# Optimization experiments

Hardware: AMD Instinct MI355X
Metric: run time of the kernel (lower is better)

The kernel has to match this reference:

```python
import jax, jax.numpy as jnp
import numpy as np

N, E, C, LMAX, NELEM = 20000, 400000, 64, 3, 10
AVG_NEIGH = 20.0


def setup_inputs() -> dict:
    key = jax.random.key(0)
    ks = jax.random.split(key, 8)
    elems = jax.random.randint(ks[0], (N,), 0, NELEM)
    node_attrs = jax.nn.one_hot(elems, NELEM, dtype=jnp.float32)  # one-hot element encoding (argmax'd by skip_tp)
    node_feats = jax.random.normal(ks[1], (N, C), dtype=jnp.float32)
    edge_attrs = jax.random.normal(ks[2], (E, (LMAX + 1) ** 2), dtype=jnp.float32)  # spherical harmonics Y_lm, lmax=3 -> 16
    edge_feats = jax.random.normal(ks[3], (E, (LMAX + 1) * C), dtype=jnp.float32)  # radial (spline) features, viewed [E, lmax+1, C]
    W_up = jax.random.normal(ks[4], (C, C), dtype=jnp.float32) / np.float32(np.sqrt(C))  # linear_matmul (pre-normalized)
    W_lin = jax.random.normal(ks[5], (LMAX + 1, C, C), dtype=jnp.float32) / np.float32(np.sqrt(C))  # per-l Linear
    W_skip = jax.random.normal(ks[6], (NELEM, LMAX + 1, C, C), dtype=jnp.float32) / np.float32(np.sqrt(C * NELEM))  # ElementalLinear
    sender = jax.random.randint(ks[7], (E,), 0, N)
    receiver = jax.random.randint(jax.random.fold_in(key, 123), (E,), 0, N)
    edge_index = jnp.stack([sender, receiver]).astype(jnp.int32)
    return dict(node_attrs=node_attrs, node_feats=node_feats, edge_attrs=edge_attrs,
                edge_feats=edge_feats, W_up=W_up, W_lin=W_lin, W_skip=W_skip,
                edge_index=edge_index)


def reference(node_attrs, node_feats, edge_attrs, edge_feats, W_up, W_lin, W_skip, edge_index):
    """InvariantInteraction of OptimizedScaleShiftInvariantMACE:
    linear_up -> InvariantMessagePassingTP (gather/TP/scatter) -> per-l linear / avg_num_neighbors
    -> elemental skip linear selected by node element (one-hot node_attrs)."""
    sender, receiver = edge_index[0], edge_index[1]
    n_nodes = node_feats.shape[0]
    n_edges = edge_feats.shape[0]

    nf = node_feats @ W_up                                   # [N, C] linear up
    ef = edge_feats.reshape(n_edges, LMAX + 1, -1)           # [E, lmax+1, C]
    sf = nf[sender]                                          # [E, C] gather sender feats

    outs = []
    for l in range(LMAX + 1):  # fixed small loop over l-blocks (structurally distinct irreps)
        sh = edge_attrs[:, l * l:(l + 1) * (l + 1)]          # [E, 2l+1]
        # per-edge tensor product: Y_lm(e) * R_l(e,c) * h(sender(e),c)
        m = sh[:, :, None] * (sf * ef[:, l, :])[:, None, :]  # [E, 2l+1, C]
        msg = jax.ops.segment_sum(m, receiver, num_segments=n_nodes)  # [N, 2l+1, C]
        msg = jnp.einsum('nmc,cd->nmd', msg, W_lin[l]) / AVG_NEIGH    # message linear
        Weff = jnp.einsum('nz,zcd->ncd', node_attrs, W_skip[:, l])    # per-node element weights
        outs.append(jnp.einsum('nmc,ncd->nmd', msg, Weff))            # elemental skip linear
    return jnp.concatenate(outs, axis=1)                     # [N, (lmax+1)^2, C]
```

## Files before the change

### kernel.cpp

```cpp
#include <hip/hip_runtime.h>

#define N_NODES 20000
#define N_EDGES 400000
#define NELEM 10
#define INV_AVG (1.0f / 20.0f)
#define NUP_BLK 5000
#define CAP 64

typedef __attribute__((ext_vector_type(8))) short short8;
typedef __attribute__((ext_vector_type(4))) float f32x4;

__device__ __forceinline__ int rlanei(int v, int l) {
    return __builtin_amdgcn_readlane(v, l);
}
__device__ __forceinline__ ushort f2bf(float x) {
    unsigned u = __float_as_uint(x);
    u += 0x7FFFu + ((u >> 16) & 1u);
    return (ushort)(u >> 16);
}
__device__ __forceinline__ float bf2f(ushort h) {
    return __uint_as_float(((unsigned)h) << 16);
}
__host__ __device__ constexpr int lOf(int lm) {
    return lm >= 9 ? 3 : lm >= 4 ? 2 : lm >= 1 ? 1 : 0;
}

__global__ void __launch_bounds__(256) k_prep(
    const float* __restrict__ node_feats,
    const float* __restrict__ W_up,
    const float* __restrict__ W_lin,
    const float* __restrict__ W_skip,
    float* __restrict__ nf,
    ushort* __restrict__ Wfrag)
{
    __shared__ float A[64 * 64];
    __shared__ float B[64 * 64];
    __shared__ float Cw[64 * 64];
    int tid = threadIdx.x;
    if (blockIdx.x < NUP_BLK) {
        for (int i = tid; i < 4096; i += 256) A[i] = W_up[i];
        __syncthreads();
        int n = blockIdx.x * 4 + (tid >> 6);
        int c = tid & 63;
        const float* row = node_feats + (size_t)n * 64;
        float acc = 0.f;
#pragma unroll
        for (int k = 0; k < 64; ++k) acc += row[k] * A[k * 64 + c];
        nf[(size_t)n * 64 + c] = acc;
    } else {
        int zl = blockIdx.x - NUP_BLK;
        int l = zl & 3;
        for (int i = tid; i < 4096; i += 256) {
            A[i] = W_lin[l * 4096 + i];
            B[i] = W_skip[zl * 4096 + i];
        }
        __syncthreads();
        for (int i = tid; i < 4096; i += 256) {
            int k = i >> 6, d = i & 63;
            float acc = 0.f;
#pragma unroll
            for (int c = 0; c < 64; ++c) acc += A[k * 64 + c] * B[c * 64 + d];
            Cw[i] = acc * INV_AVG;
        }
        __syncthreads();
        for (int fid = tid; fid < 8192; fid += 256) {
            int plane = fid >> 12;
            int rem = fid & 4095;
            int kk = rem >> 11;
            int nt = (rem >> 9) & 3;
            int ln = (rem >> 3) & 63;
            int j  = rem & 7;
            int c = kk * 32 + ((ln >> 4) << 3) + j;
            int d = nt * 16 + (ln & 15);
            float v = Cw[c * 64 + d];
            ushort hi = f2bf(v);
            ushort val = plane ? f2bf(v - bf2f(hi)) : hi;
            Wfrag[(size_t)plane * 163840 + (((size_t)zl * 2 + kk) * 4 + nt) * 512 + ln * 8 + j] = val;
        }
    }
}

__global__ void __launch_bounds__(256) k_bucket(
    const int* __restrict__ sender, const int* __restrict__ receiver,
    int* __restrict__ cnt, int2* __restrict__ slots)
{
    int e = blockIdx.x * 256 + threadIdx.x;
    if (e >= N_EDGES) return;
    int r = receiver[e];
    int p = atomicAdd(&cnt[r], 1);
    if (p < CAP) slots[(size_t)r * CAP + p] = make_int2(e, sender[e]);
}

struct Slot {
    float f0, f1, f2, f3, sh, sf;
};

__device__ __forceinline__ void refill(
    Slot& S, int eb, int sb, int idx, int lane,
    const float* __restrict__ edge_feats,
    const float* __restrict__ edge_attrs,
    const float* __restrict__ nf)
{
    int e_ = rlanei(eb, idx);
    int s_ = rlanei(sb, idx);
    const float* ef_ = edge_feats + (size_t)e_ * 256;
    S.f0 = ef_[lane];
    S.f1 = ef_[64 + lane];
    S.f2 = ef_[128 + lane];
    S.f3 = ef_[192 + lane];
    S.sh = edge_attrs[(size_t)e_ * 16 + (lane & 15)];
    S.sf = nf[(size_t)s_ * 64 + lane];
}

__device__ __forceinline__ float rlanef(float v, int l) {
    return __int_as_float(__builtin_amdgcn_readlane(__float_as_int(v), l));
}

__device__ __forceinline__ void compute(const Slot& S, float* acc)
{
    float pr0 = S.sf * S.f0, pr1 = S.sf * S.f1;
    float pr2 = S.sf * S.f2, pr3 = S.sf * S.f3;
    acc[0] += rlanef(S.sh, 0) * pr0;
#pragma unroll
    for (int lm = 1; lm < 4; ++lm)  acc[lm] += rlanef(S.sh, lm) * pr1;
#pragma unroll
    for (int lm = 4; lm < 9; ++lm)  acc[lm] += rlanef(S.sh, lm) * pr2;
#pragma unroll
    for (int lm = 9; lm < 16; ++lm) acc[lm] += rlanef(S.sh, lm) * pr3;
}

__global__ void __launch_bounds__(256) k_gather_out(
    const float* __restrict__ nf,
    const float* __restrict__ edge_attrs,
    const float* __restrict__ edge_feats,
    const float* __restrict__ node_attrs,
    const ushort* __restrict__ Wfrag,
    const int* __restrict__ cnt,
    const int2* __restrict__ slots,
    float* __restrict__ out)
{
    __shared__ __align__(16) ushort Abuf[4][2][16][64];
    int w = threadIdx.x >> 6;
    int node = blockIdx.x * 4 + w;
    int lane = threadIdx.x & 63;
    if (node >= N_NODES) return;
    int nb = min(cnt[node], CAP);

    float acc[16];
#pragma unroll
    for (int lm = 0; lm < 16; ++lm) acc[lm] = 0.f;

    if (nb > 0) {
        int2 ep = (lane < nb) ? slots[(size_t)node * CAP + lane] : make_int2(0, 0);
        int eb = ep.x, sb = ep.y;

        Slot a, b;
        refill(a, eb, sb, 0, lane, edge_feats, edge_attrs, nf);
        if (nb > 1) refill(b, eb, sb, 1, lane, edge_feats, edge_attrs, nf);

        for (int i = 0; i < nb; i += 2) {
            compute(a, acc);
            if (i + 2 < nb) refill(a, eb, sb, i + 2, lane, edge_feats, edge_attrs, nf);
            if (i + 1 < nb) compute(b, acc);
            if (i + 3 < nb) refill(b, eb, sb, i + 3, lane, edge_feats, edge_attrs, nf);
        }
    }

#pragma unroll
    for (int lm = 0; lm < 16; ++lm) {
        ushort hi = f2bf(acc[lm]);
        ushort lo = f2bf(acc[lm] - bf2f(hi));
        Abuf[w][0][lm][lane] = hi;
        Abuf[w][1][lm][lane] = lo;
    }

    int m = lane & 15;
    int g = (lane >> 4) & 3;

    short8 ah[2], al[2];
#pragma unroll
    for (int kk = 0; kk < 2; ++kk) {
        ah[kk] = *(const short8*)&Abuf[w][0][m][kk * 32 + g * 8];
        al[kk] = *(const short8*)&Abuf[w][1][m][kk * 32 + g * 8];
    }

    const float* arow = node_attrs + (size_t)node * NELEM;
    int z = 0;
#pragma unroll
    for (int j = 1; j < NELEM; ++j) if (arow[j] > 0.5f) z = j;

    f32x4 dacc[4][4];
#pragma unroll
    for (int l = 0; l < 4; ++l)
#pragma unroll
        for (int nt = 0; nt < 4; ++nt)
            dacc[l][nt] = f32x4{0.f, 0.f, 0.f, 0.f};

#pragma unroll
    for (int l = 0; l < 4; ++l) {
        size_t zl = (size_t)(z * 4 + l);
#pragma unroll
        for (int nt = 0; nt < 4; ++nt) {
#pragma unroll
            for (int kk = 0; kk < 2; ++kk) {
                const short8 bh = *(const short8*)(Wfrag + ((zl * 2 + kk) * 4 + nt) * 512 + lane * 8);
                const short8 bl = *(const short8*)(Wfrag + 163840 + ((zl * 2 + kk) * 4 + nt) * 512 + lane * 8);
                dacc[l][nt] = __builtin_amdgcn_mfma_f32_16x16x32_bf16(ah[kk], bh, dacc[l][nt], 0, 0, 0);
                dacc[l][nt] = __builtin_amdgcn_mfma_f32_16x16x32_bf16(al[kk], bh, dacc[l][nt], 0, 0, 0);
                dacc[l][nt] = __builtin_amdgcn_mfma_f32_16x16x32_bf16(ah[kk], bl, dacc[l][nt], 0, 0, 0);
            }
        }
    }

    float* ob = out + (size_t)node * 1024;
#pragma unroll
    for (int nt = 0; nt < 4; ++nt) {
#pragma unroll
        for (int r = 0; r < 4; ++r) {
            float v0 = dacc[lOf(0 + r)][nt][r];
            float v1 = dacc[lOf(4 + r)][nt][r];
            float v2 = dacc[lOf(8 + r)][nt][r];
            float v3 = dacc[lOf(12 + r)][nt][r];
            float v = (g == 0) ? v0 : (g == 1) ? v1 : (g == 2) ? v2 : v3;
            int row = g * 4 + r;
            ob[row * 64 + nt * 16 + m] = v;
        }
    }
}

extern "C" void kernel_launch(void* const* d_in, const int* in_sizes, int n_in,
                              void* d_out, int out_size, void* d_ws, size_t ws_size,
                              hipStream_t stream)
{
    const float* node_attrs = (const float*)d_in[0];
    const float* node_feats = (const float*)d_in[1];
    const float* edge_attrs = (const float*)d_in[2];
    const float* edge_feats = (const float*)d_in[3];
    const float* W_up       = (const float*)d_in[4];
    const float* W_lin      = (const float*)d_in[5];
    const float* W_skip     = (const float*)d_in[6];
    const int*   edge_index = (const int*)d_in[7];
    const int* sender   = edge_index;
    const int* receiver = edge_index + N_EDGES;
    float* out = (float*)d_out;

    int2*   slots = (int2*)d_ws;
    float*  nf    = (float*)(slots + (size_t)N_NODES * CAP);
    ushort* Wfrag = (ushort*)(nf + (size_t)N_NODES * 64);
    int*    cnt   = (int*)(Wfrag + 2 * 163840);

    hipMemsetAsync(cnt, 0, N_NODES * sizeof(int), stream);

    k_prep<<<NUP_BLK + NELEM * 4, 256, 0, stream>>>(
        node_feats, W_up, W_lin, W_skip, nf, Wfrag);
    k_bucket<<<(N_EDGES + 255) / 256, 256, 0, stream>>>(sender, receiver, cnt, slots);
    k_gather_out<<<(N_NODES + 3) / 4, 256, 0, stream>>>(
        nf, edge_attrs, edge_feats, node_attrs, Wfrag, cnt, slots, out);
}
```

Measured before the change: 240.3 us.

## Deepen edge prefetch to four slots, pad LDS rows, shrink MFMA accumulator state

The gather loop now keeps four in-flight edge slots instead of two, so more memory loads overlap with compute. The LDS staging buffer rows are padded from 64 to 72 to avoid bank conflicts. The MFMA epilogue processes one l-block at a time with a non-unrolled loop, holding 4 accumulators instead of 16 and storing through a predicate, which cuts register pressure. The linear_up prep now does 4 nodes per wave per block with fewer blocks, which lowers occupancy of that phase but gives more live Slot registers in the gather kernel.

```diff
diff --git a/kernel.cpp b/kernel.cpp
--- a/kernel.cpp
+++ b/kernel.cpp
@@ -4,7 +4,7 @@
 #define N_EDGES 400000
 #define NELEM 10
 #define INV_AVG (1.0f / 20.0f)
-#define NUP_BLK 5000
+#define NUP_BLK 1250
 #define CAP 64
 
 typedef __attribute__((ext_vector_type(8))) short short8;
@@ -12,6 +12,9 @@
 
 __device__ __forceinline__ int rlanei(int v, int l) {
     return __builtin_amdgcn_readlane(v, l);
+}
+__device__ __forceinline__ float rlanef(float v, int l) {
+    return __int_as_float(__builtin_amdgcn_readlane(__float_as_int(v), l));
 }
 __device__ __forceinline__ ushort f2bf(float x) {
     unsigned u = __float_as_uint(x);
@@ -20,9 +23,6 @@
 }
 __device__ __forceinline__ float bf2f(ushort h) {
     return __uint_as_float(((unsigned)h) << 16);
-}
-__host__ __device__ constexpr int lOf(int lm) {
-    return lm >= 9 ? 3 : lm >= 4 ? 2 : lm >= 1 ? 1 : 0;
 }
 
 __global__ void __launch_bounds__(256) k_prep(
@@ -40,13 +40,17 @@
     if (blockIdx.x < NUP_BLK) {
         for (int i = tid; i < 4096; i += 256) A[i] = W_up[i];
         __syncthreads();
-        int n = blockIdx.x * 4 + (tid >> 6);
+        int sub = tid >> 6;
         int c = tid & 63;
-        const float* row = node_feats + (size_t)n * 64;
-        float acc = 0.f;
-#pragma unroll
-        for (int k = 0; k < 64; ++k) acc += row[k] * A[k * 64 + c];
-        nf[(size_t)n * 64 + c] = acc;
+#pragma unroll
+        for (int j = 0; j < 4; ++j) {
+            int n = blockIdx.x * 16 + j * 4 + sub;
+            const float* row = node_feats + (size_t)n * 64;
+            float acc = 0.f;
+#pragma unroll
+            for (int k = 0; k < 64; ++k) acc += row[k] * A[k * 64 + c];
+            nf[(size_t)n * 64 + c] = acc;
+        }
     } else {
         int zl = blockIdx.x - NUP_BLK;
         int l = zl & 3;
@@ -112,10 +116,6 @@
     S.sf = nf[(size_t)s_ * 64 + lane];
 }
 
-__device__ __forceinline__ float rlanef(float v, int l) {
-    return __int_as_float(__builtin_amdgcn_readlane(__float_as_int(v), l));
-}
-
 __device__ __forceinline__ void compute(const Slot& S, float* acc)
 {
     float pr0 = S.sf * S.f0, pr1 = S.sf * S.f1;
@@ -139,7 +139,7 @@
     const int2* __restrict__ slots,
     float* __restrict__ out)
 {
-    __shared__ __align__(16) ushort Abuf[4][2][16][64];
+    __shared__ __align__(16) ushort Abuf[4][2][16][72];
     int w = threadIdx.x >> 6;
     int node = blockIdx.x * 4 + w;
     int lane = threadIdx.x & 63;
@@ -154,15 +154,27 @@
         int2 ep = (lane < nb) ? slots[(size_t)node * CAP + lane] : make_int2(0, 0);
         int eb = ep.x, sb = ep.y;
 
-        Slot a, b;
-        refill(a, eb, sb, 0, lane, edge_feats, edge_attrs, nf);
-        if (nb > 1) refill(b, eb, sb, 1, lane, edge_feats, edge_attrs, nf);
-
-        for (int i = 0; i < nb; i += 2) {
-            compute(a, acc);
-            if (i + 2 < nb) refill(a, eb, sb, i + 2, lane, edge_feats, edge_attrs, nf);
-            if (i + 1 < nb) compute(b, acc);
-            if (i + 3 < nb) refill(b, eb, sb, i + 3, lane, edge_feats, edge_attrs, nf);
+        Slot s0, s1, s2, s3;
+        refill(s0, eb, sb, 0, lane, edge_feats, edge_attrs, nf);
+        if (nb > 1) refill(s1, eb, sb, 1, lane, edge_feats, edge_attrs, nf);
+        if (nb > 2) refill(s2, eb, sb, 2, lane, edge_feats, edge_attrs, nf);
+        if (nb > 3) refill(s3, eb, sb, 3, lane, edge_feats, edge_attrs, nf);
+
+        for (int i = 0; i < nb; i += 4) {
+            compute(s0, acc);
+            if (i + 4 < nb) refill(s0, eb, sb, i + 4, lane, edge_feats, edge_attrs, nf);
+            if (i + 1 < nb) {
+                compute(s1, acc);
+                if (i + 5 < nb) refill(s1, eb, sb, i + 5, lane, edge_feats, edge_attrs, nf);
+            }
+            if (i + 2 < nb) {
+                compute(s2, acc);
+                if (i + 6 < nb) refill(s2, eb, sb, i + 6, lane, edge_feats, edge_attrs, nf);
+            }
+            if (i + 3 < nb) {
+                compute(s3, acc);
+                if (i + 7 < nb) refill(s3, eb, sb, i + 7, lane, edge_feats, edge_attrs, nf);
+            }
         }
     }
 
@@ -189,41 +201,33 @@
 #pragma unroll
     for (int j = 1; j < NELEM; ++j) if (arow[j] > 0.5f) z = j;
 
-    f32x4 dacc[4][4];
-#pragma unroll
-    for (int l = 0; l < 4; ++l)
-#pragma unroll
-        for (int nt = 0; nt < 4; ++nt)
-            dacc[l][nt] = f32x4{0.f, 0.f, 0.f, 0.f};
-
-#pragma unroll
+    float* ob = out + (size_t)node * 1024;
+
+#pragma unroll 1
     for (int l = 0; l < 4; ++l) {
         size_t zl = (size_t)(z * 4 + l);
+        f32x4 dacc[4];
+#pragma unroll
+        for (int nt = 0; nt < 4; ++nt) dacc[nt] = f32x4{0.f, 0.f, 0.f, 0.f};
 #pragma unroll
         for (int nt = 0; nt < 4; ++nt) {
 #pragma unroll
             for (int kk = 0; kk < 2; ++kk) {
                 const short8 bh = *(const short8*)(Wfrag + ((zl * 2 + kk) * 4 + nt) * 512 + lane * 8);
                 const short8 bl = *(const short8*)(Wfrag + 163840 + ((zl * 2 + kk) * 4 + nt) * 512 + lane * 8);
-                dacc[l][nt] = __builtin_amdgcn_mfma_f32_16x16x32_bf16(ah[kk], bh, dacc[l][nt], 0, 0, 0);
-                dacc[l][nt] = __builtin_amdgcn_mfma_f32_16x16x32_bf16(al[kk], bh, dacc[l][nt], 0, 0, 0);
-                dacc[l][nt] = __builtin_amdgcn_mfma_f32_16x16x32_bf16(ah[kk], bl, dacc[l][nt], 0, 0, 0);
-            }
-        }
-    }
-
-    float* ob = out + (size_t)node * 1024;
-#pragma unroll
-    for (int nt = 0; nt < 4; ++nt) {
-#pragma unroll
-        for (int r = 0; r < 4; ++r) {
-            float v0 = dacc[lOf(0 + r)][nt][r];
-            float v1 = dacc[lOf(4 + r)][nt][r];
-            float v2 = dacc[lOf(8 + r)][nt][r];
-            float v3 = dacc[lOf(12 + r)][nt][r];
-            float v = (g == 0) ? v0 : (g == 1) ? v1 : (g == 2) ? v2 : v3;
-            int row = g * 4 + r;
-            ob[row * 64 + nt * 16 + m] = v;
+                dacc[nt] = __builtin_amdgcn_mfma_f32_16x16x32_bf16(ah[kk], bh, dacc[nt], 0, 0, 0);
+                dacc[nt] = __builtin_amdgcn_mfma_f32_16x16x32_bf16(al[kk], bh, dacc[nt], 0, 0, 0);
+                dacc[nt] = __builtin_amdgcn_mfma_f32_16x16x32_bf16(ah[kk], bl, dacc[nt], 0, 0, 0);
+            }
+        }
+#pragma unroll
+        for (int nt = 0; nt < 4; ++nt) {
+#pragma unroll
+            for (int r = 0; r < 4; ++r) {
+                int row = g * 4 + r;
+                int lr = (row >= 9) ? 3 : (row >= 4) ? 2 : (row >= 1) ? 1 : 0;
+                if (lr == l) ob[row * 64 + nt * 16 + m] = dacc[nt][r];
+            }
         }
     }
 }
```

Result: faster. 232.2 us (-3.4%).
